# Optimization experiments

Hardware: AMD Instinct MI355X
Metric: run time of the kernel (lower is better)

The kernel has to match this reference:

```python
import jax, jax.numpy as jnp
import numpy as np

VOCAB = 50257
EMBED_DIM = 128
TOP_N = 8
B, LQ, LC = 4, 128, 65536


def setup_inputs() -> dict:
    key = jax.random.key(0)
    k1, k2, k3, k4 = jax.random.split(key, 4)
    query_tokens = jax.random.randint(k1, (B, LQ), 0, VOCAB, dtype=jnp.int32)
    context_tokens = jax.random.randint(k2, (LC,), 0, VOCAB, dtype=jnp.int32)
    emb_table = jax.random.normal(k3, (VOCAB, EMBED_DIM), dtype=jnp.float32) * 0.02
    W_score = jax.random.normal(k4, (EMBED_DIM, EMBED_DIM), dtype=jnp.float32) / np.sqrt(EMBED_DIM)
    b_score = jnp.zeros((EMBED_DIM,), dtype=jnp.float32)
    return {
        "query_tokens": query_tokens,
        "context_tokens": context_tokens,
        "emb_table": emb_table,
        "W_score": W_score,
        "b_score": b_score,
    }


def reference(query_tokens, context_tokens, emb_table, W_score, b_score):
    # --- TokenEmbedder: embedding lookups ---
    q = emb_table[query_tokens]        # [B, Lq, D]
    c = emb_table[context_tokens]      # [Lc, D]

    # --- ExploratoryMechanism: euclidean distance + top_n nearest ---
    # ||q - c||^2 = ||q||^2 + ||c||^2 - 2 q.c
    sq = (jnp.sum(q * q, axis=-1)[..., None]
          + jnp.sum(c * c, axis=-1)[None, None, :]
          - 2.0 * jnp.einsum('bqd,cd->bqc', q, c))      # [B, Lq, Lc]
    dist = jnp.sqrt(jnp.maximum(sq, 0.0) + 1e-12)
    neg_top, top_n_indices = jax.lax.top_k(-dist, TOP_N)  # smallest distances
    top_n_distances = -neg_top                             # [B, Lq, n]

    # --- gather top-n context embeddings ---
    top_n_embeddings = c[top_n_indices]                    # [B, Lq, n, D]

    # --- RAGScorer: projected dot-product score penalized by distance ---
    qp = q @ W_score + b_score                             # [B, Lq, D]
    logits = (jnp.einsum('bqd,bqnd->bqn', qp, top_n_embeddings)
              / np.sqrt(EMBED_DIM)) - top_n_distances      # [B, Lq, n]
    rag_scores = jax.nn.softmax(logits, axis=-1)           # [B, Lq, n]

    # --- QueryReconstructor: score-driven reweighting of query positions ---
    importance = jnp.max(rag_scores, axis=-1)              # [B, Lq]
    weights = jax.nn.softmax(importance, axis=-1)          # [B, Lq]
    lq = query_tokens.shape[1]
    reconstructed_query = query_tokens.astype(jnp.float32) * weights * lq
    return reconstructed_query
```

## Files before the change

kernel.cpp:

```cpp
#include <hip/hip_runtime.h>
#include <math.h>

#define D      128
#define NQ     512
#define LCTX   65536
#define TOPN   8
#define NCAND  16
#define QT     64
#define CCHUNK 512
#define CSTEP  128
#define NCH    (LCTX / CCHUNK)
#define PERCHUNK 16
#define NCANDTOT (NCH * PERCHUNK)
#define NQT    (NQ / QT)
#define NROWS  (LCTX + NQ)
#define FINF   3.0e38f

typedef __attribute__((ext_vector_type(8))) __bf16 bf16x8;
typedef __attribute__((ext_vector_type(4))) float f32x4;

static __device__ __forceinline__ unsigned pack2(float a, float b) {
  const unsigned ua = (__float_as_uint(a) + 0x8000u) >> 16;
  const unsigned ub = (__float_as_uint(b) + 0x8000u) & 0xffff0000u;
  return ua | ub;
}

__global__ __launch_bounds__(256) void pack_kernel(const int* __restrict__ ctok,
                                                   const int* __restrict__ qtok,
                                                   const float* __restrict__ emb,
                                                   unsigned short* __restrict__ cemb,
                                                   float* __restrict__ cn2) {
  const int g = threadIdx.x >> 5, l = threadIdx.x & 31;
  const int row = blockIdx.x * 8 + g;
  const int tok = (row < LCTX) ? ctok[row] : qtok[row - LCTX];
  const float4 v = *(const float4*)(emb + (size_t)tok * D + 4 * l);
  float p = v.x * v.x + v.y * v.y + v.z * v.z + v.w * v.w;
#pragma unroll
  for (int off = 16; off; off >>= 1) p += __shfl_xor(p, off, 32);
  if (l == 0 && row < LCTX) cn2[row] = p;
  const int c = l >> 1, h = l & 1;
  const int pch = c ^ (row & 7);
  uint2 pk = make_uint2(pack2(v.x, v.y), pack2(v.z, v.w));
  *(uint2*)(&cemb[(size_t)row * D + pch * 8 + h * 4]) = pk;
}

__global__ __launch_bounds__(256) void qprep_kernel(const int* __restrict__ qtok,
                                                    const float* __restrict__ emb,
                                                    const float* __restrict__ W,
                                                    const float* __restrict__ bvec,
                                                    float* __restrict__ qp) {
  __shared__ float sW[D * D];
  __shared__ float sq[8][D];
  const int tid = threadIdx.x;
  const int qb = blockIdx.x * 8;
#pragma unroll
  for (int j = 0; j < 16; ++j) {
    const int i4 = j * 256 + tid;
    *(float4*)(&sW[i4 * 4]) = *(const float4*)(W + i4 * 4);
  }
  {
    const int r = tid >> 5, l = tid & 31;
    const int tok = qtok[qb + r];
    *(float4*)(&sq[r][4 * l]) = *(const float4*)(emb + (size_t)tok * D + 4 * l);
  }
  __syncthreads();
  const int d = tid & 127, qs = tid >> 7;
  const float bv = bvec[d];
  float acc[4] = {bv, bv, bv, bv};
  for (int k = 0; k < D; ++k) {
    const float wv = sW[k * D + d];
#pragma unroll
    for (int i = 0; i < 4; ++i) acc[i] = fmaf(sq[2 * i + qs][k], wv, acc[i]);
  }
#pragma unroll
  for (int i = 0; i < 4; ++i) qp[(size_t)(qb + 2 * i + qs) * D + d] = acc[i];
}

__global__ __launch_bounds__(256, 4) void dist_topk_kernel(
    const unsigned short* __restrict__ cemb, const float* __restrict__ cn2,
    float2* __restrict__ partials) {
  __shared__ __align__(16) unsigned short sCt[CSTEP * D];
  __shared__ __align__(16) float scn2[CCHUNK];

  const int tid = threadIdx.x;
  const int wid = tid >> 6, lane = tid & 63;
  const int n = lane & 15, qq = lane >> 4;
  const int chunk = blockIdx.x, qtile = blockIdx.y;
  const int qbase = qtile * QT, cbase0 = chunk * CCHUNK;

  scn2[tid] = cn2[cbase0 + tid];
  scn2[tid + 256] = cn2[cbase0 + tid + 256];

  {
    const unsigned short* qrowbase = cemb + (size_t)(LCTX + qbase) * D;
#pragma unroll
    for (int j = 0; j < 4; ++j) {
      const int r0 = wid * 16 + j * 4;
      const unsigned short* gp = qrowbase + r0 * D + lane * 8;
      __builtin_amdgcn_global_load_lds(
          (const __attribute__((address_space(1))) unsigned int*)gp,
          (__attribute__((address_space(3))) unsigned int*)&sCt[r0 * D], 16, 0, 0);
    }
  }
  __syncthreads();

  bf16x8 bq[4];
  {
    const int rq = wid * 16 + n;
#pragma unroll
    for (int kk = 0; kk < 4; ++kk)
      bq[kk] = *(const bf16x8*)(&sCt[rq * D + 8 * ((4 * kk + qq) ^ (rq & 7))]);
  }

  float bs[4] = {FINF, FINF, FINF, FINF};
  int bi[4] = {0, 0, 0, 0};

  for (int st = 0; st < CCHUNK / CSTEP; ++st) {
    const int cb = cbase0 + st * CSTEP;
    __syncthreads();
    {
      const unsigned short* crowbase = cemb + (size_t)cb * D;
#pragma unroll
      for (int j = 0; j < 8; ++j) {
        const int r0 = wid * 32 + j * 4;
        const unsigned short* gp = crowbase + r0 * D + lane * 8;
        __builtin_amdgcn_global_load_lds(
            (const __attribute__((address_space(1))) unsigned int*)gp,
            (__attribute__((address_space(3))) unsigned int*)&sCt[r0 * D], 16, 0, 0);
      }
    }
    __syncthreads();

#pragma unroll
    for (int tt = 0; tt < 8; ++tt) {
      f32x4 acc = {0.f, 0.f, 0.f, 0.f};
      const int m = 16 * tt + n;
#pragma unroll
      for (int kk = 0; kk < 4; ++kk) {
        const bf16x8 af = *(const bf16x8*)(&sCt[m * D + 8 * ((4 * kk + qq) ^ (n & 7))]);
        acc = __builtin_amdgcn_mfma_f32_16x16x32_bf16(af, bq[kk], acc, 0, 0, 0);
      }
      const f32x4 cv = *(const f32x4*)(&scn2[st * CSTEP + 16 * tt + 4 * qq]);
      const int ibase = cb + 16 * tt + 4 * qq;
#pragma unroll
      for (int r = 0; r < 4; ++r) {
        const float v = fmaf(-2.f, acc[r], cv[r]);
        const int iv = ibase + r;
        const bool c0 = v < bs[0], c1 = v < bs[1], c2 = v < bs[2], c3 = v < bs[3];
        const float nb0 = fminf(bs[0], v);
        const float nb1 = __builtin_amdgcn_fmed3f(v, bs[0], bs[1]);
        const float nb2 = __builtin_amdgcn_fmed3f(v, bs[1], bs[2]);
        const float nb3 = __builtin_amdgcn_fmed3f(v, bs[2], bs[3]);
        const int ni0 = c0 ? iv : bi[0];
        const int ni1 = c1 ? (c0 ? bi[0] : iv) : bi[1];
        const int ni2 = c2 ? (c1 ? bi[1] : iv) : bi[2];
        const int ni3 = c3 ? (c2 ? bi[2] : iv) : bi[3];
        bs[0] = nb0; bs[1] = nb1; bs[2] = nb2; bs[3] = nb3;
        bi[0] = ni0; bi[1] = ni1; bi[2] = ni2; bi[3] = ni3;
      }
    }
  }

  const int q = qbase + wid * 16 + n;
  float2* dst = partials + (size_t)q * NCANDTOT + chunk * PERCHUNK + qq * 4;
#pragma unroll
  for (int t = 0; t < 4; ++t)
    dst[t] = make_float2(bs[t], __int_as_float(bi[t]));
}

__global__ __launch_bounds__(256) void select_kernel(
    const float2* __restrict__ partials, const int* __restrict__ qtok,
    const int* __restrict__ ctok, const float* __restrict__ emb,
    const float* __restrict__ qp, float* __restrict__ importance) {
  __shared__ double sd2[4][NCAND];
  __shared__ double sdp[4][NCAND];
  __shared__ int sid[4][NCAND];
  const int w = threadIdx.x >> 6, lane = threadIdx.x & 63;
  const int q = blockIdx.x * 4 + w;

  float v[32]; int vi[32];
  const float2* pq = partials + (size_t)q * NCANDTOT;
#pragma unroll
  for (int j = 0; j < 32; ++j) {
    const float2 cd = pq[64 * j + lane];
    v[j] = cd.x; vi[j] = __float_as_int(cd.y);
  }
  unsigned consumed = 0;
  int myc = 0;
#pragma unroll
  for (int t = 0; t < NCAND; ++t) {
    float lmin = FINF; int li = 0x7fffffff; int ls = 0;
#pragma unroll
    for (int j = 0; j < 32; ++j) {
      const bool take = !((consumed >> j) & 1u) && (v[j] < lmin);
      lmin = take ? v[j] : lmin;
      li = take ? vi[j] : li;
      ls = take ? j : ls;
    }
    float m = lmin; int pidx = li; int pwho = (lane << 5) | ls;
#pragma unroll
    for (int off = 32; off; off >>= 1) {
      const float om = __shfl_xor(m, off, 64);
      const int oi = __shfl_xor(pidx, off, 64);
      const int ow = __shfl_xor(pwho, off, 64);
      const bool better = (om < m) || (om == m && oi < pidx);
      m = better ? om : m; pidx = better ? oi : pidx; pwho = better ? ow : pwho;
    }
    if ((pwho >> 5) == lane) consumed |= 1u << (pwho & 31);
    if (lane == t) myc = pidx;
  }

  const int c = lane >> 2, sub = lane & 3;
  const int idx = __shfl(myc, c, 64);
  const int tc = ctok[idx];
  const int tq = qtok[q];
  const float* crow = emb + (size_t)tc * D + sub * 32;
  const float* qrow = emb + (size_t)tq * D + sub * 32;
  const float* prow = qp + (size_t)q * D + sub * 32;
  double dd = 0.0, pp = 0.0;
#pragma unroll
  for (int kk = 0; kk < 8; ++kk) {
    const float4 cv = *(const float4*)(crow + 4 * kk);
    const float4 qv = *(const float4*)(qrow + 4 * kk);
    const float4 pv = *(const float4*)(prow + 4 * kk);
    const double dx = (double)qv.x - (double)cv.x, dy = (double)qv.y - (double)cv.y;
    const double dz = (double)qv.z - (double)cv.z, dw = (double)qv.w - (double)cv.w;
    dd += dx * dx + dy * dy + dz * dz + dw * dw;
    pp += (double)pv.x * (double)cv.x + (double)pv.y * (double)cv.y +
          (double)pv.z * (double)cv.z + (double)pv.w * (double)cv.w;
  }
  dd += __shfl_xor(dd, 1, 64); dd += __shfl_xor(dd, 2, 64);
  pp += __shfl_xor(pp, 1, 64); pp += __shfl_xor(pp, 2, 64);
  if (sub == 0) { sd2[w][c] = dd; sdp[w][c] = pp; sid[w][c] = idx; }

  if (lane == 0) {
    bool used[NCAND];
#pragma unroll
    for (int n2 = 0; n2 < NCAND; ++n2) used[n2] = false;
    double lg[TOPN];
    for (int t = 0; t < TOPN; ++t) {
      int best = -1;
      for (int n2 = 0; n2 < NCAND; ++n2) {
        if (used[n2]) continue;
        if (best < 0 || sd2[w][n2] < sd2[w][best] ||
            (sd2[w][n2] == sd2[w][best] && sid[w][n2] < sid[w][best])) best = n2;
      }
      used[best] = true;
      lg[t] = sdp[w][best] * 0.08838834764831843 - sqrt(sd2[w][best] + 1e-12);
    }
    double m = lg[0];
#pragma unroll
    for (int t = 1; t < TOPN; ++t) m = fmax(m, lg[t]);
    double sum = 0.0;
#pragma unroll
    for (int t = 0; t < TOPN; ++t) sum += exp(lg[t] - m);
    importance[q] = (float)(1.0 / sum);
  }
}

__global__ __launch_bounds__(128) void out_kernel(const float* __restrict__ importance,
                                                  const int* __restrict__ qtok,
                                                  float* __restrict__ out) {
  const int b = blockIdx.x, i = threadIdx.x;
  __shared__ double sred[2];
  const double v = (double)importance[b * 128 + i];
  double m = v;
#pragma unroll
  for (int off = 32; off; off >>= 1) m = fmax(m, __shfl_xor(m, off, 64));
  if ((i & 63) == 0) sred[i >> 6] = m;
  __syncthreads();
  const double M = fmax(sred[0], sred[1]);
  const double e = exp(v - M);
  double s = e;
#pragma unroll
  for (int off = 32; off; off >>= 1) s += __shfl_xor(s, off, 64);
  __syncthreads();
  if ((i & 63) == 0) sred[i >> 6] = s;
  __syncthreads();
  const double S = sred[0] + sred[1];
  out[b * 128 + i] = (float)((double)qtok[b * 128 + i] * (e / S) * 128.0);
}

extern "C" void kernel_launch(void* const* d_in, const int* in_sizes, int n_in,
                              void* d_out, int out_size, void* d_ws, size_t ws_size,
                              hipStream_t stream) {
  const int* qtok = (const int*)d_in[0];
  const int* ctok = (const int*)d_in[1];
  const float* emb = (const float*)d_in[2];
  const float* W = (const float*)d_in[3];
  const float* bvec = (const float*)d_in[4];
  float* out = (float*)d_out;

  char* ws = (char*)d_ws;
  float* cn2 = (float*)ws;
  float* qp = cn2 + LCTX;
  float* imp = qp + (size_t)NQ * D;
  unsigned short* cemb = (unsigned short*)(imp + NQ);
  float2* partials = (float2*)(cemb + (size_t)NROWS * D);

  pack_kernel<<<NROWS / 8, 256, 0, stream>>>(ctok, qtok, emb, cemb, cn2);
  qprep_kernel<<<NQ / 8, 256, 0, stream>>>(qtok, emb, W, bvec, qp);
  dist_topk_kernel<<<dim3(NCH, NQT), 256, 0, stream>>>(cemb, cn2, partials);
  select_kernel<<<NQ / 4, 256, 0, stream>>>(partials, qtok, ctok, emb, qp, imp);
  out_kernel<<<4, 128, 0, stream>>>(imp, qtok, out);
}
```

Baseline: 158.2 us.

## Spread per-query candidate selection across a full 256-thread block

The select kernel now gives each query a whole block of four wavefronts instead of a single wavefront. Each wavefront picks its local 16 smallest candidates from 512 entries, and wavefront 0 merges the 64 results through shared memory. The float64 distance and projection recompute is then split across 16 lanes per candidate. This cuts the serial per-lane work and register use in select (8 entries per lane instead of 32) and launches 512 blocks instead of 128, at the cost of extra __syncthreads and a second merge pass.

```diff
diff --git a/kernel.cpp b/kernel.cpp
--- a/kernel.cpp
+++ b/kernel.cpp
@@ -172,32 +172,32 @@
     const float2* __restrict__ partials, const int* __restrict__ qtok,
     const int* __restrict__ ctok, const float* __restrict__ emb,
     const float* __restrict__ qp, float* __restrict__ importance) {
-  __shared__ double sd2[4][NCAND];
-  __shared__ double sdp[4][NCAND];
-  __shared__ int sid[4][NCAND];
-  const int w = threadIdx.x >> 6, lane = threadIdx.x & 63;
-  const int q = blockIdx.x * 4 + w;
-
-  float v[32]; int vi[32];
+  __shared__ float2 swt[64];
+  __shared__ double sd2[NCAND], sdp[NCAND];
+  __shared__ int sid[NCAND];
+  const int tid = threadIdx.x;
+  const int w = tid >> 6, lane = tid & 63;
+  const int q = blockIdx.x;
+
+  float v[8]; int vi[8];
   const float2* pq = partials + (size_t)q * NCANDTOT;
 #pragma unroll
-  for (int j = 0; j < 32; ++j) {
-    const float2 cd = pq[64 * j + lane];
+  for (int j = 0; j < 8; ++j) {
+    const float2 cd = pq[256 * j + tid];
     v[j] = cd.x; vi[j] = __float_as_int(cd.y);
   }
   unsigned consumed = 0;
-  int myc = 0;
 #pragma unroll
   for (int t = 0; t < NCAND; ++t) {
     float lmin = FINF; int li = 0x7fffffff; int ls = 0;
 #pragma unroll
-    for (int j = 0; j < 32; ++j) {
+    for (int j = 0; j < 8; ++j) {
       const bool take = !((consumed >> j) & 1u) && (v[j] < lmin);
       lmin = take ? v[j] : lmin;
       li = take ? vi[j] : li;
       ls = take ? j : ls;
     }
-    float m = lmin; int pidx = li; int pwho = (lane << 5) | ls;
+    float m = lmin; int pidx = li; int pwho = (lane << 3) | ls;
 #pragma unroll
     for (int off = 32; off; off >>= 1) {
       const float om = __shfl_xor(m, off, 64);
@@ -206,20 +206,44 @@
       const bool better = (om < m) || (om == m && oi < pidx);
       m = better ? om : m; pidx = better ? oi : pidx; pwho = better ? ow : pwho;
     }
-    if ((pwho >> 5) == lane) consumed |= 1u << (pwho & 31);
-    if (lane == t) myc = pidx;
-  }
-
-  const int c = lane >> 2, sub = lane & 3;
-  const int idx = __shfl(myc, c, 64);
+    if ((pwho >> 3) == lane) consumed |= 1u << (pwho & 7);
+    if (lane == t) swt[w * 16 + t] = make_float2(m, __int_as_float(pidx));
+  }
+  __syncthreads();
+
+  if (w == 0) {
+    const float2 cd = swt[lane];
+    const float mv = cd.x; const int mi = __float_as_int(cd.y);
+    bool cons = false;
+#pragma unroll
+    for (int t = 0; t < NCAND; ++t) {
+      float m = cons ? FINF : mv;
+      int pidx = cons ? 0x7fffffff : mi;
+      int pwho = lane;
+#pragma unroll
+      for (int off = 32; off; off >>= 1) {
+        const float om = __shfl_xor(m, off, 64);
+        const int oi = __shfl_xor(pidx, off, 64);
+        const int ow = __shfl_xor(pwho, off, 64);
+        const bool better = (om < m) || (om == m && oi < pidx);
+        m = better ? om : m; pidx = better ? oi : pidx; pwho = better ? ow : pwho;
+      }
+      if (pwho == lane) cons = true;
+      if (lane == t) sid[t] = pidx;
+    }
+  }
+  __syncthreads();
+
+  const int c = tid >> 4, sub = tid & 15;
+  const int idx = sid[c];
   const int tc = ctok[idx];
   const int tq = qtok[q];
-  const float* crow = emb + (size_t)tc * D + sub * 32;
-  const float* qrow = emb + (size_t)tq * D + sub * 32;
-  const float* prow = qp + (size_t)q * D + sub * 32;
+  const float* crow = emb + (size_t)tc * D + sub * 8;
+  const float* qrow = emb + (size_t)tq * D + sub * 8;
+  const float* prow = qp + (size_t)q * D + sub * 8;
   double dd = 0.0, pp = 0.0;
 #pragma unroll
-  for (int kk = 0; kk < 8; ++kk) {
+  for (int kk = 0; kk < 2; ++kk) {
     const float4 cv = *(const float4*)(crow + 4 * kk);
     const float4 qv = *(const float4*)(qrow + 4 * kk);
     const float4 pv = *(const float4*)(prow + 4 * kk);
@@ -229,11 +253,15 @@
     pp += (double)pv.x * (double)cv.x + (double)pv.y * (double)cv.y +
           (double)pv.z * (double)cv.z + (double)pv.w * (double)cv.w;
   }
-  dd += __shfl_xor(dd, 1, 64); dd += __shfl_xor(dd, 2, 64);
-  pp += __shfl_xor(pp, 1, 64); pp += __shfl_xor(pp, 2, 64);
-  if (sub == 0) { sd2[w][c] = dd; sdp[w][c] = pp; sid[w][c] = idx; }
-
-  if (lane == 0) {
+#pragma unroll
+  for (int off = 1; off <= 8; off <<= 1) {
+    dd += __shfl_xor(dd, off, 64);
+    pp += __shfl_xor(pp, off, 64);
+  }
+  if (sub == 0) { sd2[c] = dd; sdp[c] = pp; }
+  __syncthreads();
+
+  if (tid == 0) {
     bool used[NCAND];
 #pragma unroll
     for (int n2 = 0; n2 < NCAND; ++n2) used[n2] = false;
@@ -242,11 +270,11 @@
       int best = -1;
       for (int n2 = 0; n2 < NCAND; ++n2) {
         if (used[n2]) continue;
-        if (best < 0 || sd2[w][n2] < sd2[w][best] ||
-            (sd2[w][n2] == sd2[w][best] && sid[w][n2] < sid[w][best])) best = n2;
+        if (best < 0 || sd2[n2] < sd2[best] ||
+            (sd2[n2] == sd2[best] && sid[n2] < sid[best])) best = n2;
       }
       used[best] = true;
-      lg[t] = sdp[w][best] * 0.08838834764831843 - sqrt(sd2[w][best] + 1e-12);
+      lg[t] = sdp[best] * 0.08838834764831843 - sqrt(sd2[best] + 1e-12);
     }
     double m = lg[0];
 #pragma unroll
@@ -301,6 +329,6 @@
   pack_kernel<<<NROWS / 8, 256, 0, stream>>>(ctok, qtok, emb, cemb, cn2);
   qprep_kernel<<<NQ / 8, 256, 0, stream>>>(qtok, emb, W, bvec, qp);
   dist_topk_kernel<<<dim3(NCH, NQT), 256, 0, stream>>>(cemb, cn2, partials);
-  select_kernel<<<NQ / 4, 256, 0, stream>>>(partials, qtok, ctok, emb, qp, imp);
+  select_kernel<<<NQ, 256, 0, stream>>>(partials, qtok, ctok, emb, qp, imp);
   out_kernel<<<4, 128, 0, stream>>>(imp, qtok, out);
 }
```

After: 150.8 us. -4.7%, faster.
